# Performance work log

Hardware: AMD Instinct MI355X
Metric: run time of the kernel (lower is better)

## Reference

```python
import jax, jax.numpy as jnp
import numpy as np

N, D_IN, D_H, D_OUT, M = 256, 768, 768, 512, 100000


def setup_inputs() -> dict:
    key = jax.random.key(0)
    ks = jax.random.split(key, 8)
    img_feats = jax.random.normal(ks[0], (N, D_IN), dtype=jnp.float32)
    w1 = jax.random.normal(ks[1], (D_H, D_IN), dtype=jnp.float32) * (1.0 / np.sqrt(D_IN))
    b1 = jax.random.normal(ks[2], (D_H,), dtype=jnp.float32) * 0.01
    w2 = jax.random.normal(ks[3], (D_OUT, D_H), dtype=jnp.float32) * (1.0 / np.sqrt(D_H))
    b2 = jax.random.normal(ks[4], (D_OUT,), dtype=jnp.float32) * 0.01
    logit_scale = jnp.asarray(np.log(1.0 / 0.07), dtype=jnp.float32)
    loc = jax.random.normal(ks[5], (M, D_OUT), dtype=jnp.float32)
    loc_feats = loc / jnp.linalg.norm(loc, axis=1, keepdims=True)  # pre-normalized gallery
    gps_gallery = jax.random.uniform(ks[6], (M, 2), dtype=jnp.float32, minval=-90.0, maxval=90.0)
    return {
        "img_feats": img_feats, "w1": w1, "b1": b1, "w2": w2, "b2": b2,
        "logit_scale": logit_scale, "loc_feats": loc_feats,
        "gps_gallery": gps_gallery, "top_k": 5,
    }


def reference(img_feats, w1, b1, w2, b2, logit_scale, loc_feats, gps_gallery, top_k):
    # Tsfm MLP head: Linear -> ReLU -> Linear
    h = jax.nn.relu(img_feats @ w1.T + b1)            # [N, D_H]
    img = h @ w2.T + b2                               # [N, D_OUT]
    # F.normalize(dim=1)
    img_n = img / jnp.linalg.norm(img, axis=1, keepdims=True)
    # forward_cached: scaled cosine-similarity logits against 100K gallery
    logits = jnp.exp(logit_scale) * (img_n @ loc_feats.T)  # [N, M]
    # predict: softmax over full gallery row, then top-k retrieval
    probs = jax.nn.softmax(logits, axis=-1)
    top_vals, top_idx = jax.lax.top_k(probs, top_k)   # [N, k]
    top_pred_gps = gps_gallery[top_idx[0]]            # [k, 2] (first image, as in original)
    top_pred_prob = top_vals[0]                       # [k]
    return (logits, top_pred_gps, top_pred_prob)
```

## Files before the change

### kernel.cpp

```cpp
#include <hip/hip_runtime.h>
#include <math.h>

#define N_IMG 256
#define DIN   768
#define DH    768
#define DOUT  512
#define M_GAL 100000
#define CAP   2048

typedef __bf16 bf16_t;
typedef __bf16 bf16x8 __attribute__((ext_vector_type(8)));
typedef __bf16 bf16x4 __attribute__((ext_vector_type(4)));
typedef float  f32x4  __attribute__((ext_vector_type(4)));

#define OFF_H      0
#define OFF_IMG    (N_IMG*DH)
#define OFF_IMGN   (OFF_IMG  + N_IMG*DOUT)
#define OFF_IMGBF  (OFF_IMGN + N_IMG*DOUT)
#define OFF_STATS  (OFF_IMGBF + N_IMG*DOUT/2)
#define OFF_CIDX   (OFF_STATS + 4)
#define OFF_CVAL   (OFF_CIDX + CAP)

#define OUT_GPS  ((size_t)N_IMG * (size_t)M_GAL)
#define OUT_PROB (OUT_GPS + 10)

__device__ inline unsigned fkey(float x) {
  unsigned u = __float_as_uint(x);
  return (u & 0x80000000u) ? ~u : (u | 0x80000000u);
}
__device__ inline float fkey_inv(unsigned k) {
  unsigned u = (k & 0x80000000u) ? (k ^ 0x80000000u) : ~k;
  return __uint_as_float(u);
}

template<int KDIM, int NCOLS, bool RELU>
__global__ __launch_bounds__(256) void mlp_gemm(const float* __restrict__ A,
    const float* __restrict__ B, const float* __restrict__ bias,
    float* __restrict__ C, unsigned* stats_init) {
  if (stats_init && blockIdx.x == 0 && blockIdx.y == 0 && threadIdx.x == 0) {
    stats_init[0] = 0u; stats_init[1] = 0u; stats_init[2] = 0u;
  }
  __shared__ float As[32][34];
  __shared__ float Bs[32][34];
  const int t  = threadIdx.x;
  const int rowbase = blockIdx.y * 32;
  const int colbase = blockIdx.x * 32;
  const int sm = t >> 3;
  const int kc = (t & 7) << 2;
  const int ty = t >> 4, tx = t & 15;
  float a00 = 0.f, a01 = 0.f, a10 = 0.f, a11 = 0.f;
  for (int kt = 0; kt < KDIM; kt += 32) {
    float4 av = *(const float4*)(A + (size_t)(rowbase + sm) * KDIM + kt + kc);
    float4 bv = *(const float4*)(B + (size_t)(colbase + sm) * KDIM + kt + kc);
    __syncthreads();
    As[kc+0][sm] = av.x; As[kc+1][sm] = av.y; As[kc+2][sm] = av.z; As[kc+3][sm] = av.w;
    Bs[kc+0][sm] = bv.x; Bs[kc+1][sm] = bv.y; Bs[kc+2][sm] = bv.z; Bs[kc+3][sm] = bv.w;
    __syncthreads();
#pragma unroll
    for (int j = 0; j < 32; ++j) {
      float2 a = *(const float2*)(&As[j][2*ty]);
      float2 b = *(const float2*)(&Bs[j][2*tx]);
      a00 = fmaf(a.x, b.x, a00); a01 = fmaf(a.x, b.y, a01);
      a10 = fmaf(a.y, b.x, a10); a11 = fmaf(a.y, b.y, a11);
    }
  }
  const int r0 = rowbase + 2*ty;
  const int c0 = colbase + 2*tx;
  const float bb0 = bias[c0], bb1 = bias[c0+1];
  float v00 = a00 + bb0, v01 = a01 + bb1, v10 = a10 + bb0, v11 = a11 + bb1;
  if (RELU) {
    v00 = fmaxf(v00, 0.f); v01 = fmaxf(v01, 0.f);
    v10 = fmaxf(v10, 0.f); v11 = fmaxf(v11, 0.f);
  }
  C[(size_t)r0*NCOLS + c0]       = v00; C[(size_t)r0*NCOLS + c0 + 1]     = v01;
  C[(size_t)(r0+1)*NCOLS + c0]   = v10; C[(size_t)(r0+1)*NCOLS + c0 + 1] = v11;
}

__global__ __launch_bounds__(256) void norm_cast_kernel(const float* __restrict__ img,
    float* __restrict__ img_n, bf16_t* __restrict__ img_bf) {
  const int row = blockIdx.x, t = threadIdx.x;
  const float v0 = img[row*DOUT + t];
  const float v1 = img[row*DOUT + 256 + t];
  float s = v0*v0 + v1*v1;
  for (int o = 32; o > 0; o >>= 1) s += __shfl_down(s, o);
  __shared__ float ws4[4];
  if ((t & 63) == 0) ws4[t >> 6] = s;
  __syncthreads();
  const float tot = ws4[0] + ws4[1] + ws4[2] + ws4[3];
  const float inv = 1.0f / sqrtf(tot);
  const float n0 = v0 * inv, n1 = v1 * inv;
  img_n[row*DOUT + t]        = n0;
  img_n[row*DOUT + 256 + t]  = n1;
  img_bf[row*DOUT + t]       = (bf16_t)n0;
  img_bf[row*DOUT + 256 + t] = (bf16_t)n1;
}

__global__ __launch_bounds__(256) void logits_kernel(const float* __restrict__ loc,
    const bf16_t* __restrict__ img_bf, const float* __restrict__ ls,
    float* __restrict__ out) {
  __shared__ bf16_t Al[128 * 32];
  __shared__ bf16_t Bl[128 * 40];
  const int t = threadIdx.x;
  const int w = t >> 6, l = t & 63;
  const int bx = blockIdx.x;
  const int mtile = (bx >> 4) * 8 + (bx & 7);
  const int ntile = (bx >> 3) & 1;
  const int mb = mtile * 128;
  const int nb = ntile * 128;
  const int wn = (w >> 1) * 64;
  const int wm = (w & 1) * 64;
  const int lr = l & 15, lq = l >> 4;
  f32x4 acc[4][4];
#pragma unroll
  for (int i = 0; i < 4; ++i)
#pragma unroll
    for (int j = 0; j < 4; ++j)
      acc[i][j] = (f32x4){0.f, 0.f, 0.f, 0.f};

  const int srow = t >> 3;
  const int skc  = (t & 7) << 2;

  for (int kt = 0; kt < 512; kt += 32) {
    __syncthreads();
#pragma unroll
    for (int r = 0; r < 2; ++r) {
      const int chunk = r*256 + w*64 + l;
      const int row = chunk >> 2;
      const int ko  = (chunk & 3) << 3;
      __builtin_amdgcn_global_load_lds(
          (__attribute__((address_space(1))) void*)(img_bf + (size_t)(nb + row)*512 + kt + ko),
          (__attribute__((address_space(3))) void*)(Al + (r*256 + w*64)*8),
          16, 0, 0);
    }
#pragma unroll
    for (int i = 0; i < 4; ++i) {
      const int row = i*32 + srow;
      const int gr = mb + row;
      float4 f = make_float4(0.f, 0.f, 0.f, 0.f);
      if (gr < M_GAL) f = *(const float4*)(loc + (size_t)gr*512 + kt + skc);
      bf16x4 bv;
      bv[0] = (bf16_t)f.x; bv[1] = (bf16_t)f.y; bv[2] = (bf16_t)f.z; bv[3] = (bf16_t)f.w;
      *(bf16x4*)(Bl + row*40 + skc) = bv;
    }
    __syncthreads();
    bf16x8 af[4], bfr[4];
#pragma unroll
    for (int i = 0; i < 4; ++i)
      af[i] = *(const bf16x8*)(Al + (wn + i*16 + lr)*32 + lq*8);
#pragma unroll
    for (int j = 0; j < 4; ++j)
      bfr[j] = *(const bf16x8*)(Bl + (wm + j*16 + lr)*40 + lq*8);
#pragma unroll
    for (int i = 0; i < 4; ++i)
#pragma unroll
      for (int j = 0; j < 4; ++j)
        acc[i][j] = __builtin_amdgcn_mfma_f32_16x16x32_bf16(af[i], bfr[j], acc[i][j], 0, 0, 0);
  }
  const float scale = expf(ls[0]);
#pragma unroll
  for (int i = 0; i < 4; ++i) {
    const int imgr = nb + wn + i*16 + lq*4;
#pragma unroll
    for (int j = 0; j < 4; ++j) {
      const int gal = mb + wm + j*16 + lr;
      if (gal < M_GAL) {
        const size_t base = (size_t)imgr * M_GAL + gal;
#pragma unroll
        for (int r = 0; r < 4; ++r)
          out[base + (size_t)r * M_GAL] = scale * acc[i][j][r];
      }
    }
  }
}

__global__ __launch_bounds__(256) void row0_stats(const float* __restrict__ out,
    float* __restrict__ sumexp, unsigned* __restrict__ maxkey) {
  const int i = blockIdx.x * 256 + threadIdx.x;
  float v = -1e30f, e = 0.f;
  if (i < M_GAL) { v = out[i]; e = expf(v); }
  for (int o = 32; o > 0; o >>= 1) {
    v = fmaxf(v, __shfl_down(v, o));
    e += __shfl_down(e, o);
  }
  __shared__ float wm4[4], ws4[4];
  const int t = threadIdx.x;
  if ((t & 63) == 0) { wm4[t>>6] = v; ws4[t>>6] = e; }
  __syncthreads();
  if (t == 0) {
    const float mv = fmaxf(fmaxf(wm4[0], wm4[1]), fmaxf(wm4[2], wm4[3]));
    const float sv = ws4[0] + ws4[1] + ws4[2] + ws4[3];
    atomicAdd(sumexp, sv);
    atomicMax(maxkey, fkey(mv));
  }
}

__global__ __launch_bounds__(256) void collect_kernel(const float* __restrict__ out,
    const unsigned* __restrict__ maxkey, unsigned* __restrict__ counter,
    int* __restrict__ cidx) {
  const int i = blockIdx.x * 256 + threadIdx.x;
  if (i >= M_GAL) return;
  const float thresh = fkey_inv(*maxkey) - 0.8f;
  if (out[i] > thresh) {
    const unsigned p = atomicAdd(counter, 1u);
    if (p < CAP) cidx[p] = i;
  }
}

__global__ __launch_bounds__(256) void recompute_kernel(const float* __restrict__ loc,
    const float* __restrict__ img_n, const float* __restrict__ ls,
    const unsigned* __restrict__ counter, const int* __restrict__ cidx,
    float* __restrict__ cval) {
  const int w = threadIdx.x >> 6, l = threadIdx.x & 63;
  const unsigned cnt = *counter;
  const int n = (int)(cnt < CAP ? cnt : CAP);
  const float scale = expf(ls[0]);
  for (int c = blockIdx.x * 4 + w; c < n; c += gridDim.x * 4) {
    const int idx = cidx[c];
    const float* B = loc + (size_t)idx * 512;
    float s = 0.f;
#pragma unroll
    for (int e = 0; e < 8; ++e) s = fmaf(img_n[l + e*64], B[l + e*64], s);
    for (int o = 32; o > 0; o >>= 1) s += __shfl_down(s, o);
    if (l == 0) cval[c] = scale * s;
  }
}

__global__ __launch_bounds__(256) void finalize_kernel(const unsigned* __restrict__ counter,
    const int* __restrict__ cidx, const float* __restrict__ cval,
    const float* __restrict__ gps, const float* __restrict__ sumexp,
    float* __restrict__ out) {
  __shared__ float v[CAP];
  __shared__ int   id[CAP];
  __shared__ float rv[256];
  __shared__ int   ri[256];
  __shared__ int   rs[256];
  const int t = threadIdx.x;
  const unsigned cnt = *counter;
  const int n = (int)(cnt < CAP ? cnt : CAP);
  for (int i = t; i < CAP; i += 256) {
    v[i]  = (i < n) ? cval[i] : -1e30f;
    id[i] = (i < n) ? cidx[i] : 0x7fffffff;
  }
  const float se = *sumexp;
  __syncthreads();
  for (int k = 0; k < 5; ++k) {
    float bv = -1e30f; int bidx = 0x7fffffff; int bslot = -1;
    for (int i = t; i < CAP; i += 256) {
      const float vi = v[i]; const int ii = id[i];
      if (vi > bv || (vi == bv && ii < bidx)) { bv = vi; bidx = ii; bslot = i; }
    }
    rv[t] = bv; ri[t] = bidx; rs[t] = bslot;
    __syncthreads();
    for (int s = 128; s > 0; s >>= 1) {
      if (t < s) {
        if (rv[t+s] > rv[t] || (rv[t+s] == rv[t] && ri[t+s] < ri[t])) {
          rv[t] = rv[t+s]; ri[t] = ri[t+s]; rs[t] = rs[t+s];
        }
      }
      __syncthreads();
    }
    if (t == 0) {
      const int sl = rs[0]; const int gi = ri[0]; const float lv = rv[0];
      float g0 = 0.f, g1 = 0.f, pr = 0.f;
      if (sl >= 0 && gi != 0x7fffffff) {
        g0 = gps[(size_t)gi*2]; g1 = gps[(size_t)gi*2 + 1];
        pr = expf(lv) / se;
        v[sl] = -1e30f; id[sl] = 0x7fffffff;
      }
      out[OUT_GPS + 2*k]     = g0;
      out[OUT_GPS + 2*k + 1] = g1;
      out[OUT_PROB + k]      = pr;
    }
    __syncthreads();
  }
}

extern "C" void kernel_launch(void* const* d_in, const int* in_sizes, int n_in,
                              void* d_out, int out_size, void* d_ws, size_t ws_size,
                              hipStream_t stream) {
  const float* img_feats = (const float*)d_in[0];
  const float* w1  = (const float*)d_in[1];
  const float* b1  = (const float*)d_in[2];
  const float* w2  = (const float*)d_in[3];
  const float* b2  = (const float*)d_in[4];
  const float* ls  = (const float*)d_in[5];
  const float* loc = (const float*)d_in[6];
  const float* gps = (const float*)d_in[7];
  float* out = (float*)d_out;
  float* ws  = (float*)d_ws;

  float*   h       = ws + OFF_H;
  float*   img     = ws + OFF_IMG;
  float*   img_n   = ws + OFF_IMGN;
  bf16_t*  img_bf  = (bf16_t*)(ws + OFF_IMGBF);
  float*   sumexp  = ws + OFF_STATS;
  unsigned* maxkey = (unsigned*)(ws + OFF_STATS + 1);
  unsigned* counter= (unsigned*)(ws + OFF_STATS + 2);
  int*     cidx    = (int*)(ws + OFF_CIDX);
  float*   cval    = ws + OFF_CVAL;

  mlp_gemm<DIN, DH, true><<<dim3(DH/32, N_IMG/32), 256, 0, stream>>>(
      img_feats, w1, b1, h, (unsigned*)(ws + OFF_STATS));
  mlp_gemm<DH, DOUT, false><<<dim3(DOUT/32, N_IMG/32), 256, 0, stream>>>(
      h, w2, b2, img, nullptr);
  norm_cast_kernel<<<N_IMG, 256, 0, stream>>>(img, img_n, img_bf);
  logits_kernel<<<1568, 256, 0, stream>>>(loc, img_bf, ls, out);
  const int nb391 = (M_GAL + 255) / 256;
  row0_stats<<<nb391, 256, 0, stream>>>(out, sumexp, maxkey);
  collect_kernel<<<nb391, 256, 0, stream>>>(out, maxkey, counter, cidx);
  recompute_kernel<<<128, 256, 0, stream>>>(loc, img_n, ls, counter, cidx, cval);
  finalize_kernel<<<1, 256, 0, stream>>>(counter, cidx, cval, gps, sumexp, out);
}
```

Baseline: 496.5 us.

## Restructure logits GEMM to stream gallery from registers, fuse row-0 softmax stats

The logits kernel now preloads the whole 64-image by 512-K bf16 activation tile into LDS once, using an image layout transposed in norm_cast. Each wave reads gallery rows straight from global into registers and converts them to bf16 fragments, removing the per-K-step LDS staging and barriers. Row-0 max and sum-exp are computed in the GEMM epilogue, which drops the row0_stats kernel. The recompute and finalize kernels are merged into one block. The risks are global loads with no LDS reuse across waves for the gallery operand, a single-block recompute that may be slow, and gallery reads repeated across the four N-tiles.

```diff
diff --git a/kernel.cpp b/kernel.cpp
--- a/kernel.cpp
+++ b/kernel.cpp
@@ -7,19 +7,18 @@
 #define DOUT  512
 #define M_GAL 100000
 #define CAP   2048
+#define MT    392
 
 typedef __bf16 bf16_t;
 typedef __bf16 bf16x8 __attribute__((ext_vector_type(8)));
-typedef __bf16 bf16x4 __attribute__((ext_vector_type(4)));
 typedef float  f32x4  __attribute__((ext_vector_type(4)));
 
 #define OFF_H      0
 #define OFF_IMG    (N_IMG*DH)
 #define OFF_IMGN   (OFF_IMG  + N_IMG*DOUT)
-#define OFF_IMGBF  (OFF_IMGN + N_IMG*DOUT)
-#define OFF_STATS  (OFF_IMGBF + N_IMG*DOUT/2)
+#define OFF_IMGT   (OFF_IMGN + N_IMG*DOUT)
+#define OFF_STATS  (OFF_IMGT + N_IMG*DOUT/2)
 #define OFF_CIDX   (OFF_STATS + 4)
-#define OFF_CVAL   (OFF_CIDX + CAP)
 
 #define OUT_GPS  ((size_t)N_IMG * (size_t)M_GAL)
 #define OUT_PROB (OUT_GPS + 10)
@@ -77,7 +76,7 @@
 }
 
 __global__ __launch_bounds__(256) void norm_cast_kernel(const float* __restrict__ img,
-    float* __restrict__ img_n, bf16_t* __restrict__ img_bf) {
+    float* __restrict__ img_n, bf16_t* __restrict__ img_t) {
   const int row = blockIdx.x, t = threadIdx.x;
   const float v0 = img[row*DOUT + t];
   const float v1 = img[row*DOUT + 256 + t];
@@ -89,27 +88,37 @@
   const float tot = ws4[0] + ws4[1] + ws4[2] + ws4[3];
   const float inv = 1.0f / sqrtf(tot);
   const float n0 = v0 * inv, n1 = v1 * inv;
-  img_n[row*DOUT + t]        = n0;
-  img_n[row*DOUT + 256 + t]  = n1;
-  img_bf[row*DOUT + t]       = (bf16_t)n0;
-  img_bf[row*DOUT + 256 + t] = (bf16_t)n1;
+  img_n[row*DOUT + t]       = n0;
+  img_n[row*DOUT + 256 + t] = n1;
+  const int k0 = t, k1 = t + 256;
+  img_t[(((k0 >> 3)*N_IMG) + row)*8 + (k0 & 7)] = (bf16_t)n0;
+  img_t[(((k1 >> 3)*N_IMG) + row)*8 + (k1 & 7)] = (bf16_t)n1;
 }
 
 __global__ __launch_bounds__(256) void logits_kernel(const float* __restrict__ loc,
-    const bf16_t* __restrict__ img_bf, const float* __restrict__ ls,
-    float* __restrict__ out) {
-  __shared__ bf16_t Al[128 * 32];
-  __shared__ bf16_t Bl[128 * 40];
+    const bf16_t* __restrict__ img_t, const float* __restrict__ ls,
+    float* __restrict__ out, float* __restrict__ sumexp, unsigned* __restrict__ maxkey) {
+  __shared__ bf16_t Asl[64 * 64 * 8];
   const int t = threadIdx.x;
   const int w = t >> 6, l = t & 63;
   const int bx = blockIdx.x;
-  const int mtile = (bx >> 4) * 8 + (bx & 7);
-  const int ntile = (bx >> 3) & 1;
-  const int mb = mtile * 128;
-  const int nb = ntile * 128;
-  const int wn = (w >> 1) * 64;
-  const int wm = (w & 1) * 64;
+  const int mtile = (bx & 7) + (bx >> 5) * 8;
+  const int ntile = (bx >> 3) & 3;
+  const int mb = mtile * 256;
+  const int nb = ntile * 64;
+
+#pragma unroll
+  for (int r = 0; r < 16; ++r) {
+    const int c = r * 4 + w;
+    __builtin_amdgcn_global_load_lds(
+        (__attribute__((address_space(1))) void*)(img_t + ((size_t)c * N_IMG + nb + l) * 8),
+        (__attribute__((address_space(3))) void*)(Asl + (c * 64 + l) * 8),
+        16, 0, 0);
+  }
+  __syncthreads();
+
   const int lr = l & 15, lq = l >> 4;
+  const int mw = mb + w * 64;
   f32x4 acc[4][4];
 #pragma unroll
   for (int i = 0; i < 4; ++i)
@@ -117,52 +126,66 @@
     for (int j = 0; j < 4; ++j)
       acc[i][j] = (f32x4){0.f, 0.f, 0.f, 0.f};
 
-  const int srow = t >> 3;
-  const int skc  = (t & 7) << 2;
-
-  for (int kt = 0; kt < 512; kt += 32) {
-    __syncthreads();
-#pragma unroll
-    for (int r = 0; r < 2; ++r) {
-      const int chunk = r*256 + w*64 + l;
-      const int row = chunk >> 2;
-      const int ko  = (chunk & 3) << 3;
-      __builtin_amdgcn_global_load_lds(
-          (__attribute__((address_space(1))) void*)(img_bf + (size_t)(nb + row)*512 + kt + ko),
-          (__attribute__((address_space(3))) void*)(Al + (r*256 + w*64)*8),
-          16, 0, 0);
-    }
-#pragma unroll
-    for (int i = 0; i < 4; ++i) {
-      const int row = i*32 + srow;
-      const int gr = mb + row;
-      float4 f = make_float4(0.f, 0.f, 0.f, 0.f);
-      if (gr < M_GAL) f = *(const float4*)(loc + (size_t)gr*512 + kt + skc);
-      bf16x4 bv;
-      bv[0] = (bf16_t)f.x; bv[1] = (bf16_t)f.y; bv[2] = (bf16_t)f.z; bv[3] = (bf16_t)f.w;
-      *(bf16x4*)(Bl + row*40 + skc) = bv;
-    }
-    __syncthreads();
-    bf16x8 af[4], bfr[4];
+  int mrow[4];
+#pragma unroll
+  for (int j = 0; j < 4; ++j) {
+    int m = mw + j * 16 + lr;
+    mrow[j] = m < M_GAL ? m : (M_GAL - 1);
+  }
+
+#pragma unroll 2
+  for (int kt = 0; kt < 16; ++kt) {
+    float4 b0[4], b1[4];
+#pragma unroll
+    for (int j = 0; j < 4; ++j) {
+      const float* p = loc + (size_t)mrow[j] * 512 + kt * 32 + lq * 8;
+      b0[j] = *(const float4*)p;
+      b1[j] = *(const float4*)(p + 4);
+    }
+    bf16x8 af[4];
 #pragma unroll
     for (int i = 0; i < 4; ++i)
-      af[i] = *(const bf16x8*)(Al + (wn + i*16 + lr)*32 + lq*8);
-#pragma unroll
-    for (int j = 0; j < 4; ++j)
-      bfr[j] = *(const bf16x8*)(Bl + (wm + j*16 + lr)*40 + lq*8);
-#pragma unroll
-    for (int i = 0; i < 4; ++i)
-#pragma unroll
-      for (int j = 0; j < 4; ++j)
-        acc[i][j] = __builtin_amdgcn_mfma_f32_16x16x32_bf16(af[i], bfr[j], acc[i][j], 0, 0, 0);
-  }
+      af[i] = *(const bf16x8*)(Asl + ((kt * 4 + lq) * 64 + i * 16 + lr) * 8);
+#pragma unroll
+    for (int j = 0; j < 4; ++j) {
+      bf16x8 bfr;
+      bfr[0] = (bf16_t)b0[j].x; bfr[1] = (bf16_t)b0[j].y;
+      bfr[2] = (bf16_t)b0[j].z; bfr[3] = (bf16_t)b0[j].w;
+      bfr[4] = (bf16_t)b1[j].x; bfr[5] = (bf16_t)b1[j].y;
+      bfr[6] = (bf16_t)b1[j].z; bfr[7] = (bf16_t)b1[j].w;
+#pragma unroll
+      for (int i = 0; i < 4; ++i)
+        acc[i][j] = __builtin_amdgcn_mfma_f32_16x16x32_bf16(af[i], bfr, acc[i][j], 0, 0, 0);
+    }
+  }
+
   const float scale = expf(ls[0]);
+  if (ntile == 0) {
+    float mx = -1e30f, se = 0.f;
+    if (lq == 0) {
+#pragma unroll
+      for (int j = 0; j < 4; ++j) {
+        const int m = mw + j * 16 + lr;
+        if (m < M_GAL) {
+          const float v = scale * acc[0][j][0];
+          mx = fmaxf(mx, v);
+          se += expf(v);
+        }
+      }
+    }
+#pragma unroll
+    for (int o = 1; o < 64; o <<= 1) {
+      mx = fmaxf(mx, __shfl_xor(mx, o));
+      se += __shfl_xor(se, o);
+    }
+    if (l == 0) { atomicAdd(sumexp, se); atomicMax(maxkey, fkey(mx)); }
+  }
 #pragma unroll
   for (int i = 0; i < 4; ++i) {
-    const int imgr = nb + wn + i*16 + lq*4;
+    const int imgr = nb + i * 16 + lq * 4;
 #pragma unroll
     for (int j = 0; j < 4; ++j) {
-      const int gal = mb + wm + j*16 + lr;
+      const int gal = mw + j * 16 + lr;
       if (gal < M_GAL) {
         const size_t base = (size_t)imgr * M_GAL + gal;
 #pragma unroll
@@ -170,27 +193,6 @@
           out[base + (size_t)r * M_GAL] = scale * acc[i][j][r];
       }
     }
-  }
-}
-
-__global__ __launch_bounds__(256) void row0_stats(const float* __restrict__ out,
-    float* __restrict__ sumexp, unsigned* __restrict__ maxkey) {
-  const int i = blockIdx.x * 256 + threadIdx.x;
-  float v = -1e30f, e = 0.f;
-  if (i < M_GAL) { v = out[i]; e = expf(v); }
-  for (int o = 32; o > 0; o >>= 1) {
-    v = fmaxf(v, __shfl_down(v, o));
-    e += __shfl_down(e, o);
-  }
-  __shared__ float wm4[4], ws4[4];
-  const int t = threadIdx.x;
-  if ((t & 63) == 0) { wm4[t>>6] = v; ws4[t>>6] = e; }
-  __syncthreads();
-  if (t == 0) {
-    const float mv = fmaxf(fmaxf(wm4[0], wm4[1]), fmaxf(wm4[2], wm4[3]));
-    const float sv = ws4[0] + ws4[1] + ws4[2] + ws4[3];
-    atomicAdd(sumexp, sv);
-    atomicMax(maxkey, fkey(mv));
   }
 }
 
@@ -206,27 +208,9 @@
   }
 }
 
-__global__ __launch_bounds__(256) void recompute_kernel(const float* __restrict__ loc,
+__global__ __launch_bounds__(256) void final_kernel(const float* __restrict__ loc,
     const float* __restrict__ img_n, const float* __restrict__ ls,
     const unsigned* __restrict__ counter, const int* __restrict__ cidx,
-    float* __restrict__ cval) {
-  const int w = threadIdx.x >> 6, l = threadIdx.x & 63;
-  const unsigned cnt = *counter;
-  const int n = (int)(cnt < CAP ? cnt : CAP);
-  const float scale = expf(ls[0]);
-  for (int c = blockIdx.x * 4 + w; c < n; c += gridDim.x * 4) {
-    const int idx = cidx[c];
-    const float* B = loc + (size_t)idx * 512;
-    float s = 0.f;
-#pragma unroll
-    for (int e = 0; e < 8; ++e) s = fmaf(img_n[l + e*64], B[l + e*64], s);
-    for (int o = 32; o > 0; o >>= 1) s += __shfl_down(s, o);
-    if (l == 0) cval[c] = scale * s;
-  }
-}
-
-__global__ __launch_bounds__(256) void finalize_kernel(const unsigned* __restrict__ counter,
-    const int* __restrict__ cidx, const float* __restrict__ cval,
     const float* __restrict__ gps, const float* __restrict__ sumexp,
     float* __restrict__ out) {
   __shared__ float v[CAP];
@@ -234,12 +218,26 @@
   __shared__ float rv[256];
   __shared__ int   ri[256];
   __shared__ int   rs[256];
+  __shared__ float a0[DOUT];
   const int t = threadIdx.x;
   const unsigned cnt = *counter;
   const int n = (int)(cnt < CAP ? cnt : CAP);
-  for (int i = t; i < CAP; i += 256) {
-    v[i]  = (i < n) ? cval[i] : -1e30f;
-    id[i] = (i < n) ? cidx[i] : 0x7fffffff;
+  const float scale = expf(ls[0]);
+  a0[t] = img_n[t]; a0[t + 256] = img_n[t + 256];
+  __syncthreads();
+  for (int c = t; c < CAP; c += 256) {
+    if (c < n) {
+      const int gi = cidx[c];
+      const float* B = loc + (size_t)gi * 512;
+      float s = 0.f;
+#pragma unroll 8
+      for (int k = 0; k < 512; k += 4) {
+        const float4 b = *(const float4*)(B + k);
+        s = fmaf(a0[k], b.x, s); s = fmaf(a0[k+1], b.y, s);
+        s = fmaf(a0[k+2], b.z, s); s = fmaf(a0[k+3], b.w, s);
+      }
+      v[c] = scale * s; id[c] = gi;
+    } else { v[c] = -1e30f; id[c] = 0x7fffffff; }
   }
   const float se = *sumexp;
   __syncthreads();
@@ -289,25 +287,21 @@
   float* out = (float*)d_out;
   float* ws  = (float*)d_ws;
 
-  float*   h       = ws + OFF_H;
-  float*   img     = ws + OFF_IMG;
-  float*   img_n   = ws + OFF_IMGN;
-  bf16_t*  img_bf  = (bf16_t*)(ws + OFF_IMGBF);
-  float*   sumexp  = ws + OFF_STATS;
-  unsigned* maxkey = (unsigned*)(ws + OFF_STATS + 1);
-  unsigned* counter= (unsigned*)(ws + OFF_STATS + 2);
-  int*     cidx    = (int*)(ws + OFF_CIDX);
-  float*   cval    = ws + OFF_CVAL;
+  float*    h       = ws + OFF_H;
+  float*    img     = ws + OFF_IMG;
+  float*    img_n   = ws + OFF_IMGN;
+  bf16_t*   img_t   = (bf16_t*)(ws + OFF_IMGT);
+  float*    sumexp  = ws + OFF_STATS;
+  unsigned* maxkey  = (unsigned*)(ws + OFF_STATS + 1);
+  unsigned* counter = (unsigned*)(ws + OFF_STATS + 2);
+  int*      cidx    = (int*)(ws + OFF_CIDX);
 
   mlp_gemm<DIN, DH, true><<<dim3(DH/32, N_IMG/32), 256, 0, stream>>>(
       img_feats, w1, b1, h, (unsigned*)(ws + OFF_STATS));
   mlp_gemm<DH, DOUT, false><<<dim3(DOUT/32, N_IMG/32), 256, 0, stream>>>(
       h, w2, b2, img, nullptr);
-  norm_cast_kernel<<<N_IMG, 256, 0, stream>>>(img, img_n, img_bf);
-  logits_kernel<<<1568, 256, 0, stream>>>(loc, img_bf, ls, out);
-  const int nb391 = (M_GAL + 255) / 256;
-  row0_stats<<<nb391, 256, 0, stream>>>(out, sumexp, maxkey);
-  collect_kernel<<<nb391, 256, 0, stream>>>(out, maxkey, counter, cidx);
-  recompute_kernel<<<128, 256, 0, stream>>>(loc, img_n, ls, counter, cidx, cval);
-  finalize_kernel<<<1, 256, 0, stream>>>(counter, cidx, cval, gps, sumexp, out);
-}
+  norm_cast_kernel<<<N_IMG, 256, 0, stream>>>(img, img_n, img_t);
+  logits_kernel<<<MT * 4, 256, 0, stream>>>(loc, img_t, ls, out, sumexp, maxkey);
+  collect_kernel<<<(M_GAL + 255) / 256, 256, 0, stream>>>(out, maxkey, counter, cidx);
+  final_kernel<<<1, 256, 0, stream>>>(loc, img_n, ls, counter, cidx, gps, sumexp, out);
+}
```

Measured after the change: 481.3 us. 3.1% less time.
